# Kernel optimization log

Hardware: AMD Instinct MI355X
Metric: run time of the kernel (lower is better)

The kernel has to match this reference:

```python
import jax, jax.numpy as jnp
import numpy as np

NUM_HOPS = 4
N_NODES = 50000
N_EDGES = 500000
D = 128
H1 = 256
INIT_A, INIT_B = -0.01, 0.01


def _mlp(x, w1, b1, w2, b2):
    # Linear -> ReLU -> Linear -> ReLU (Dropout is identity in eval mode)
    h = jax.nn.relu(x @ w1 + b1)
    return jax.nn.relu(h @ w2 + b2)


def _uniform(key, shape):
    return jax.random.uniform(key, shape, jnp.float32, INIT_A, INIT_B)


def setup_inputs() -> dict:
    key = jax.random.key(0)
    ks = jax.random.split(key, 40)
    inp = {
        "batch_token": jax.random.normal(ks[0], (N_NODES, D), jnp.float32),
        "edge_p_node": jax.random.randint(ks[1], (N_EDGES,), 0, N_NODES),
        "edge_c_node": jax.random.randint(ks[2], (N_EDGES,), 0, N_NODES),
        "edge_p_indicate": jax.random.uniform(ks[3], (N_EDGES,), jnp.float32),
        "edge_c_indicate": jax.random.uniform(ks[4], (N_EDGES,), jnp.float32),
        "p_mask": jax.random.uniform(ks[5], (N_NODES,), jnp.float32),
        "c_mask": jax.random.uniform(ks[6], (N_NODES,), jnp.float32),
        "start_token": jax.random.normal(ks[7], (D,), jnp.float32),
        "end_token": jax.random.normal(ks[8], (D,), jnp.float32),
    }
    # MLP_V: D -> H1 -> D ; MLP_E: 1 -> H1 -> D ; MLP_p/c/aggr: 3D -> H1 -> D
    k = 9
    for name, din in (("V", D), ("E", 1), ("P", 3 * D), ("C", 3 * D), ("A", 3 * D)):
        inp[name + "w1"] = _uniform(ks[k], (din, H1)); k += 1
        inp[name + "b1"] = _uniform(ks[k], (H1,)); k += 1
        inp[name + "w2"] = _uniform(ks[k], (H1, D)); k += 1
        inp[name + "b2"] = _uniform(ks[k], (D,)); k += 1
    return inp


def reference(batch_token, edge_p_node, edge_c_node, edge_p_indicate,
              edge_c_indicate, p_mask, c_mask, start_token, end_token,
              Vw1, Vb1, Vw2, Vb2, Ew1, Eb1, Ew2, Eb2,
              Pw1, Pb1, Pw2, Pb2, Cw1, Cb1, Cw2, Cb2,
              Aw1, Ab1, Aw2, Ab2):
    n = batch_token.shape[0]
    h = _mlp(batch_token, Vw1, Vb1, Vw2, Vb2)  # [N, D]
    edge_p = _mlp(edge_p_indicate[:, None], Ew1, Eb1, Ew2, Eb2)  # [E, D]
    edge_c = _mlp(edge_c_indicate[:, None], Ew1, Eb1, Ew2, Eb2)  # [E, D]
    ones_e = jnp.ones((edge_p_node.shape[0],), jnp.float32)
    cnt_p = jnp.clip(jax.ops.segment_sum(ones_e, edge_p_node, num_segments=n), 1.0)
    cnt_c = jnp.clip(jax.ops.segment_sum(ones_e, edge_c_node, num_segments=n), 1.0)
    for _ in range(NUM_HOPS - 1):
        hp = h[edge_p_node]  # [E, D]
        hc = h[edge_c_node]  # [E, D]
        s_p = _mlp(jnp.concatenate([hc, hp, edge_p], -1), Pw1, Pb1, Pw2, Pb2)
        s_c = _mlp(jnp.concatenate([hp, hc, edge_c], -1), Cw1, Cb1, Cw2, Cb2)
        s_p = jax.ops.segment_sum(s_p, edge_p_node, num_segments=n) / cnt_p[:, None]
        s_c = jax.ops.segment_sum(s_c, edge_c_node, num_segments=n) / cnt_c[:, None]
        s_p = s_p + p_mask[:, None] * start_token
        s_c = s_c + c_mask[:, None] * end_token
        x_aggr = jnp.concatenate([h, s_p, s_c], -1)  # [N, 3D]
        h = jax.nn.relu(h + _mlp(x_aggr, Aw1, Ab1, Aw2, Ab2))
    return h
```

## Files before the change

### kernel.cpp

```cpp
#include <hip/hip_runtime.h>
#include <hip/hip_bf16.h>
#include <cstdint>
#include <cstddef>
#include <cmath>

typedef __bf16 bf16;
typedef bf16 bf16x8 __attribute__((ext_vector_type(8)));
typedef float f32x4 __attribute__((ext_vector_type(4)));

#define D_DIM 128
#define NB 32
#define EB 128
#define TS 136
#define XS 264
#define SRS 132
#define AS 392

__device__ __forceinline__ f32x4 mfma16(bf16x8 a, bf16x8 b, f32x4 c) {
  return __builtin_amdgcn_mfma_f32_16x16x32_bf16(a, b, c, 0, 0, 0);
}

__device__ __forceinline__ int clampi(int v, int hi) {
  return v < 0 ? 0 : (v > hi ? hi : v);
}

__device__ __forceinline__ void stage16(const float* __restrict__ src, bf16* dst) {
  bf16 tmp[16];
#pragma unroll
  for (int q = 0; q < 4; ++q) {
    f32x4 f = ((const f32x4*)src)[q];
#pragma unroll
    for (int j = 0; j < 4; ++j) tmp[q * 4 + j] = (bf16)f[j];
  }
  *(bf16x8*)dst = *(bf16x8*)tmp;
  *(bf16x8*)(dst + 8) = *(bf16x8*)(tmp + 8);
}

template <int NSEG>
__device__ __forceinline__ void mlp_layer1(const bf16* s0, const bf16* s1, const bf16* s2,
                                           const int S,
                                           const bf16* __restrict__ W1t,
                                           const float* __restrict__ B1,
                                           bf16* x2, const int lane, const int w) {
  const int col = lane & 15, quad = lane >> 4;
  const int K = NSEG * 128;
  f32x4 acc[2][4] = {};
  const bf16* segs[3] = {s0, s1, s2};
#pragma unroll
  for (int sg = 0; sg < NSEG; ++sg) {
    const bf16* xl = segs[sg];
#pragma unroll
    for (int kk = 0; kk < 128; kk += 32) {
      const int k0 = sg * 128 + kk;
      bf16x8 a0 = *(const bf16x8*)&xl[col * S + kk + quad * 8];
      bf16x8 a1 = *(const bf16x8*)&xl[(col + 16) * S + kk + quad * 8];
#pragma unroll
      for (int nt = 0; nt < 4; ++nt) {
        bf16x8 b = *(const bf16x8*)(W1t + (size_t)(w * 64 + nt * 16 + col) * K + k0 + quad * 8);
        acc[0][nt] = mfma16(a0, b, acc[0][nt]);
        acc[1][nt] = mfma16(a1, b, acc[1][nt]);
      }
    }
  }
#pragma unroll
  for (int nt = 0; nt < 4; ++nt) {
    const int n = w * 64 + nt * 16 + col;
    const float b1 = B1[n];
#pragma unroll
    for (int mt = 0; mt < 2; ++mt)
#pragma unroll
      for (int i = 0; i < 4; ++i) {
        float v = acc[mt][nt][i] + b1;
        x2[(mt * 16 + quad * 4 + i) * XS + n] = (bf16)(v > 0.f ? v : 0.f);
      }
  }
}

__device__ __forceinline__ void mlp_layer2(const bf16* x2, const bf16* __restrict__ W2t,
                                           const int lane, const int w, f32x4 acc2[2][2]) {
  const int col = lane & 15, quad = lane >> 4;
#pragma unroll
  for (int k0 = 0; k0 < 256; k0 += 32) {
    bf16x8 a0 = *(const bf16x8*)&x2[col * XS + k0 + quad * 8];
    bf16x8 a1 = *(const bf16x8*)&x2[(col + 16) * XS + k0 + quad * 8];
#pragma unroll
    for (int nt = 0; nt < 2; ++nt) {
      bf16x8 b = *(const bf16x8*)(W2t + (size_t)(w * 32 + nt * 16 + col) * 256 + k0 + quad * 8);
      acc2[0][nt] = mfma16(a0, b, acc2[0][nt]);
      acc2[1][nt] = mfma16(a1, b, acc2[1][nt]);
    }
  }
}

__device__ __forceinline__ void emit_z(const bf16* x, const int S,
                                       const bf16* __restrict__ Pw1t,
                                       const bf16* __restrict__ Cw1t,
                                       bf16* __restrict__ Zbuf,
                                       const int r0, const int N,
                                       const int lane, const int w) {
  const int col = lane & 15, quad = lane >> 4;
  const bf16* base = ((w & 2) ? Cw1t : Pw1t) + (w & 1) * 128;
  bf16* out = Zbuf + (size_t)w * ((size_t)N * 256);
#pragma unroll
  for (int half = 0; half < 2; ++half) {
    f32x4 acc[2][8] = {};
#pragma unroll
    for (int kc = 0; kc < 4; ++kc) {
      bf16x8 a0 = *(const bf16x8*)&x[col * S + kc * 32 + quad * 8];
      bf16x8 a1 = *(const bf16x8*)&x[(col + 16) * S + kc * 32 + quad * 8];
#pragma unroll
      for (int nt = 0; nt < 8; ++nt) {
        const int n = half * 128 + nt * 16 + col;
        bf16x8 b = *(const bf16x8*)(base + (size_t)n * 384 + kc * 32 + quad * 8);
        acc[0][nt] = mfma16(a0, b, acc[0][nt]);
        acc[1][nt] = mfma16(a1, b, acc[1][nt]);
      }
    }
#pragma unroll
    for (int nt = 0; nt < 8; ++nt) {
      const int n = half * 128 + nt * 16 + col;
#pragma unroll
      for (int mt = 0; mt < 2; ++mt)
#pragma unroll
        for (int i = 0; i < 4; ++i) {
          int g = r0 + mt * 16 + quad * 4 + i;
          if (g < N) out[(size_t)g * 256 + n] = (bf16)acc[mt][nt][i];
        }
    }
  }
}


__global__ void transpose_kernel(const float* __restrict__ in, bf16* __restrict__ out,
                                 int K, int N) {
  int k = blockIdx.x * blockDim.x + threadIdx.x;
  int n = blockIdx.y;
  if (k < K) out[(size_t)n * K + k] = (bf16)in[(size_t)k * N + n];
}

__global__ void count_kernel(const int* __restrict__ epn, const int* __restrict__ ecn,
                             int* cntp, int* cntc, int E, int N) {
  int i = blockIdx.x * blockDim.x + threadIdx.x;
  if (i < E) {
    atomicAdd(&cntp[clampi(epn[i], N - 1)], 1);
    atomicAdd(&cntc[clampi(ecn[i], N - 1)], 1);
  }
}

__global__ void inv_kernel(const int* __restrict__ cntp, const int* __restrict__ cntc,
                           float* invp, float* invc, int N) {
  int i = blockIdx.x * blockDim.x + threadIdx.x;
  if (i < N) {
    invp[i] = 1.f / fmaxf((float)cntp[i], 1.f);
    invc[i] = 1.f / fmaxf((float)cntc[i], 1.f);
  }
}

__global__ void scan_pair_kernel(const int* __restrict__ cntp, const int* __restrict__ cntc,
                                 int* __restrict__ offp, int* __restrict__ offc, int n) {
  const int* cnt = blockIdx.x ? cntc : cntp;
  int* offs = blockIdx.x ? offc : offp;
  __shared__ int buf[1024];
  __shared__ int carry;
  const int t = threadIdx.x;
  if (t == 0) carry = 0;
  __syncthreads();
  for (int base = 0; base < n; base += 1024) {
    int v = (base + t < n) ? cnt[base + t] : 0;
    buf[t] = v;
    __syncthreads();
    for (int d = 1; d < 1024; d <<= 1) {
      int add = (t >= d) ? buf[t - d] : 0;
      __syncthreads();
      buf[t] += add;
      __syncthreads();
    }
    if (base + t < n) offs[base + t] = carry + buf[t] - v;
    __syncthreads();
    if (t == 1023) carry += buf[1023];
    __syncthreads();
  }
}

__global__ void scatter_kernel(const int* __restrict__ epn, const int* __restrict__ ecn,
                               const int* __restrict__ offp, const int* __restrict__ offc,
                               int* curp, int* curc, int* sortp, int* sortc, int E, int N) {
  int i = blockIdx.x * blockDim.x + threadIdx.x;
  if (i < E) {
    int p = clampi(epn[i], N - 1);
    sortp[offp[p] + atomicAdd(&curp[p], 1)] = i;
    int c = clampi(ecn[i], N - 1);
    sortc[offc[c] + atomicAdd(&curc[c], 1)] = i;
  }
}


__global__ __launch_bounds__(256) void emlp_table_kernel(
    const float* __restrict__ Ew1, const float* __restrict__ Eb1,
    const float* __restrict__ Ew2, const float* __restrict__ Eb2,
    float* __restrict__ ts_out, float* __restrict__ Atab, float* __restrict__ Btab) {
  __shared__ float s_tk[256], s_w[256], s_b[256];
  __shared__ int s_k[256];
  __shared__ float sA[256], sB[256];
  const int j = blockIdx.x;
  const int t = threadIdx.x;
  float w = Ew1[t], b = Eb1[t];
  float tk = (w != 0.f) ? (-b / w) : INFINITY;
  s_tk[t] = tk; s_w[t] = w; s_b[t] = b;
  __syncthreads();
  int rank = 0;
  for (int u = 0; u < 256; ++u) {
    float tu = s_tk[u];
    if (tu < tk || (tu == tk && u < t)) ++rank;
  }
  s_k[rank] = t;
  if (j == 0) ts_out[rank] = tk;
  float w2own = Ew2[(size_t)t * 128 + j];
  bool act = (w < 0.f || (w == 0.f && b > 0.f));
  sA[t] = act ? w * w2own : 0.f;
  sB[t] = act ? b * w2own : 0.f;
  __syncthreads();
  for (int d = 128; d > 0; d >>= 1) {
    if (t < d) { sA[t] += sA[t + d]; sB[t] += sB[t + d]; }
    __syncthreads();
  }
  const float baseA = sA[0], baseB = sB[0];
  __syncthreads();
  int k = s_k[t];
  float wk = s_w[k], bk = s_b[k];
  float dA = 0.f, dB = 0.f;
  if (wk != 0.f) {
    float w2 = Ew2[(size_t)k * 128 + j];
    float sgn = wk > 0.f ? 1.f : -1.f;
    dA = sgn * wk * w2;
    dB = sgn * bk * w2;
  }
  sA[t] = dA; sB[t] = dB;
  __syncthreads();
  for (int d = 1; d < 256; d <<= 1) {
    float aA = (t >= d) ? sA[t - d] : 0.f;
    float aB = (t >= d) ? sB[t - d] : 0.f;
    __syncthreads();
    sA[t] += aA; sB[t] += aB;
    __syncthreads();
  }
  const float eb2 = Eb2[j];
  if (t == 0) { Atab[j] = baseA; Btab[j] = baseB + eb2; }
  Atab[(size_t)(t + 1) * 128 + j] = baseA + sA[t];
  Btab[(size_t)(t + 1) * 128 + j] = baseB + sB[t] + eb2;
}


__global__ __launch_bounds__(256, 3) void node_v_kernel(
    const float* __restrict__ bt, const bf16* __restrict__ W1t, const float* __restrict__ B1,
    const bf16* __restrict__ W2t, const float* __restrict__ B2,
    const bf16* __restrict__ Pw1t, const bf16* __restrict__ Cw1t,
    bf16* __restrict__ Zbuf, float* __restrict__ hout, int N) {
  __shared__ __attribute__((aligned(16))) bf16 x[NB * TS];
  __shared__ __attribute__((aligned(16))) bf16 x2[NB * XS];
  const int t = threadIdx.x;
  const int r0 = blockIdx.x * NB;
  {
    const int r = t >> 3, c0 = (t & 7) * 16;
    int g = r0 + r; if (g >= N) g = N - 1;
    stage16(bt + (size_t)g * D_DIM + c0, &x[r * TS + c0]);
  }
  __syncthreads();
  const int lane = t & 63, w = t >> 6, col = lane & 15, quad = lane >> 4;
  mlp_layer1<1>(x, x, x, TS, W1t, B1, x2, lane, w);
  __syncthreads();
  f32x4 acc2[2][2] = {};
  mlp_layer2(x2, W2t, lane, w, acc2);
  __syncthreads();
#pragma unroll
  for (int nt = 0; nt < 2; ++nt) {
    const int n = w * 32 + nt * 16 + col;
    const float b2 = B2[n];
#pragma unroll
    for (int mt = 0; mt < 2; ++mt)
#pragma unroll
      for (int i = 0; i < 4; ++i) {
        int m = mt * 16 + quad * 4 + i;
        int g = r0 + m;
        float v = acc2[mt][nt][i] + b2;
        v = v > 0.f ? v : 0.f;
        x[m * TS + n] = (bf16)v;
        if (g < N) hout[(size_t)g * D_DIM + n] = v;
      }
  }
  __syncthreads();
  emit_z(x, TS, Pw1t, Cw1t, Zbuf, r0, N, lane, w);
}


__global__ __launch_bounds__(1024, 8) void edge_side_kernel(
    const bf16* __restrict__ Zbuf,
    const float* __restrict__ epi, const float* __restrict__ eci,
    const int* __restrict__ epn, const int* __restrict__ ecn,
    const int* __restrict__ sortp, const int* __restrict__ sortc,
    const float* __restrict__ ets, const float* __restrict__ Atab,
    const float* __restrict__ Btab,
    const bf16* __restrict__ Pw1t, const float* __restrict__ Pb1,
    const bf16* __restrict__ Pw2t, const float* __restrict__ Pb2,
    const bf16* __restrict__ Cw1t, const float* __restrict__ Cb1,
    const bf16* __restrict__ Cw2t, const float* __restrict__ Cb2,
    float* __restrict__ accp, float* __restrict__ accc, int E, int N) {
  const int side = blockIdx.y;
  const size_t NZ = (size_t)N * 256;
  const bf16* ZO     = Zbuf + (size_t)(side * 2 + 0) * NZ;
  const bf16* ZW     = Zbuf + (size_t)(side * 2 + 1) * NZ;
  const float* ei    = side ? eci : epi;
  const int* own_n   = side ? ecn : epn;
  const int* oth_n   = side ? epn : ecn;
  const int* sorted  = side ? sortc : sortp;
  const bf16* W1c    = (side ? Cw1t : Pw1t) + 256;
  const float* B1    = side ? Cb1 : Pb1;
  const bf16* W2t    = side ? Cw2t : Pw2t;
  const float* B2    = side ? Cb2 : Pb2;
  float* acc         = side ? accc : accp;

  __shared__ int s_own[EB], s_oth[EB];
  __shared__ float s_x[EB];
  __shared__ float s_ts[256];
  __shared__ __attribute__((aligned(16))) char ubuf[EB * TS * 2 * 2];
  bf16* feat = (bf16*)ubuf;
  bf16* xzh  = (bf16*)(ubuf + EB * TS * 2);
  float* sred = (float*)ubuf;

  const int t = threadIdx.x;
  const int e0 = blockIdx.x * EB;
  if (t < 256) s_ts[t] = ets[t];
  if (t < EB) {
    int e = e0 + t;
    if (e < E) {
      int id = clampi(sorted[e], E - 1);
      s_own[t] = clampi(own_n[id], N - 1);
      s_oth[t] = clampi(oth_n[id], N - 1);
      s_x[t] = ei[id];
    } else {
      s_own[t] = -1; s_oth[t] = 0; s_x[t] = 0.f;
    }
  }
  __syncthreads();

  const int lane = t & 63, w = t >> 6, col = lane & 15, quad = lane >> 4;
  const int zr = t >> 3, zc = (t & 7) * 16;

  const bf16* zo_row;
  const bf16* zw_row;
  bf16x8 va[2];
  {
    int ro = s_oth[zr];
    int rw = s_own[zr]; if (rw < 0) rw = 0;
    zo_row = ZO + (size_t)ro * 256;
    zw_row = ZW + (size_t)rw * 256;
#pragma unroll
    for (int q = 0; q < 2; ++q) va[q] = *(const bf16x8*)(zo_row + zc + q * 8);
  }

  {
    const float xv = s_x[zr];
    int lo = 0, hi = 256;
#pragma unroll
    for (int it = 0; it < 8; ++it) {
      int mid = (lo + hi) >> 1;
      if (s_ts[mid] < xv) lo = mid + 1; else hi = mid;
    }
    const float* Ar = Atab + (size_t)lo * 128 + zc;
    const float* Br = Btab + (size_t)lo * 128 + zc;
#pragma unroll
    for (int q = 0; q < 2; ++q) {
      f32x4 a0 = *(const f32x4*)(Ar + q * 8);
      f32x4 a1 = *(const f32x4*)(Ar + q * 8 + 4);
      f32x4 b0 = *(const f32x4*)(Br + q * 8);
      f32x4 b1v = *(const f32x4*)(Br + q * 8 + 4);
      bf16 o[8];
#pragma unroll
      for (int j = 0; j < 4; ++j) {
        float v0 = fmaf(xv, a0[j], b0[j]);
        float v1 = fmaf(xv, a1[j], b1v[j]);
        o[j] = (bf16)(v0 > 0.f ? v0 : 0.f);
        o[4 + j] = (bf16)(v1 > 0.f ? v1 : 0.f);
      }
      *(bf16x8*)&feat[zr * TS + zc + q * 8] = *(bf16x8*)o;
    }
  }

  {
#pragma unroll
    for (int q = 0; q < 2; ++q) {
      bf16x8 b = *(const bf16x8*)(zw_row + zc + q * 8);
      bf16 o[8];
#pragma unroll
      for (int j = 0; j < 8; ++j) o[j] = (bf16)((float)va[q][j] + (float)b[j]);
      *(bf16x8*)&xzh[zr * TS + zc + q * 8] = *(bf16x8*)o;
    }
  }
  __syncthreads();

#pragma unroll
  for (int q = 0; q < 2; ++q) va[q] = *(const bf16x8*)(zo_row + 128 + zc + q * 8);

  f32x4 acc2[4];
#pragma unroll
  for (int g = 0; g < 4; ++g) acc2[g] = (f32x4){0.f, 0.f, 0.f, 0.f};

  const int nh = (w & 7) * 16 + col;
  const int rbase = (w >> 3) * 64;

  {
    f32x4 acc1[4] = {};
#pragma unroll
    for (int kc = 0; kc < 4; ++kc) {
      bf16x8 b = *(const bf16x8*)(W1c + (size_t)nh * 384 + kc * 32 + quad * 8);
#pragma unroll
      for (int g = 0; g < 4; ++g) {
        bf16x8 afr = *(const bf16x8*)&feat[(rbase + g * 16 + col) * TS + kc * 32 + quad * 8];
        acc1[g] = mfma16(afr, b, acc1[g]);
      }
    }
    const float b1v = B1[nh];
#pragma unroll
    for (int g = 0; g < 4; ++g)
#pragma unroll
      for (int i = 0; i < 4; ++i) {
        const int m = rbase + g * 16 + quad * 4 + i;
        float v = acc1[g][i] + b1v + (float)xzh[m * TS + nh];
        xzh[m * TS + nh] = (bf16)(v > 0.f ? v : 0.f);
      }
  }
  __syncthreads();
#pragma unroll
  for (int kc = 0; kc < 4; ++kc) {
    bf16x8 b = *(const bf16x8*)(W2t + (size_t)nh * 256 + kc * 32 + quad * 8);
#pragma unroll
    for (int g = 0; g < 4; ++g) {
      bf16x8 afr = *(const bf16x8*)&xzh[(rbase + g * 16 + col) * TS + kc * 32 + quad * 8];
      acc2[g] = mfma16(afr, b, acc2[g]);
    }
  }
  __syncthreads();

  {
#pragma unroll
    for (int q = 0; q < 2; ++q) {
      bf16x8 b = *(const bf16x8*)(zw_row + 128 + zc + q * 8);
      bf16 o[8];
#pragma unroll
      for (int j = 0; j < 8; ++j) o[j] = (bf16)((float)va[q][j] + (float)b[j]);
      *(bf16x8*)&xzh[zr * TS + zc + q * 8] = *(bf16x8*)o;
    }
  }
  __syncthreads();

  {
    f32x4 acc1[4] = {};
#pragma unroll
    for (int kc = 0; kc < 4; ++kc) {
      bf16x8 b = *(const bf16x8*)(W1c + (size_t)(128 + nh) * 384 + kc * 32 + quad * 8);
#pragma unroll
      for (int g = 0; g < 4; ++g) {
        bf16x8 afr = *(const bf16x8*)&feat[(rbase + g * 16 + col) * TS + kc * 32 + quad * 8];
        acc1[g] = mfma16(afr, b, acc1[g]);
      }
    }
    const float b1v = B1[128 + nh];
#pragma unroll
    for (int g = 0; g < 4; ++g)
#pragma unroll
      for (int i = 0; i < 4; ++i) {
        const int m = rbase + g * 16 + quad * 4 + i;
        float v = acc1[g][i] + b1v + (float)xzh[m * TS + nh];
        xzh[m * TS + nh] = (bf16)(v > 0.f ? v : 0.f);
      }
  }
  __syncthreads();
#pragma unroll
  for (int kc = 0; kc < 4; ++kc) {
    bf16x8 b = *(const bf16x8*)(W2t + (size_t)nh * 256 + 128 + kc * 32 + quad * 8);
#pragma unroll
    for (int g = 0; g < 4; ++g) {
      bf16x8 afr = *(const bf16x8*)&xzh[(rbase + g * 16 + col) * TS + kc * 32 + quad * 8];
      acc2[g] = mfma16(afr, b, acc2[g]);
    }
  }
  __syncthreads();

  {
    const float b2 = B2[nh];
#pragma unroll
    for (int g = 0; g < 4; ++g)
#pragma unroll
      for (int i = 0; i < 4; ++i) {
        float v = acc2[g][i] + b2;
        sred[(rbase + g * 16 + quad * 4 + i) * SRS + nh] = v > 0.f ? v : 0.f;
      }
  }
  __syncthreads();
  {
    const int c = t & 127;
    const int rlo = (t >> 7) * 16;
    float run = 0.f;
    int cur = s_own[rlo];
    for (int r = rlo; r < rlo + 16; ++r) {
      int k = s_own[r];
      if (k != cur) {
        if (cur >= 0)
          __hip_atomic_fetch_add(&acc[(size_t)cur * D_DIM + c], run,
                                 __ATOMIC_RELAXED, __HIP_MEMORY_SCOPE_AGENT);
        run = 0.f;
        cur = k;
      }
      run += sred[r * SRS + c];
    }
    if (cur >= 0)
      __hip_atomic_fetch_add(&acc[(size_t)cur * D_DIM + c], run,
                             __ATOMIC_RELAXED, __HIP_MEMORY_SCOPE_AGENT);
  }
}


__global__ __launch_bounds__(256, 3) void node_a_kernel(
    const float* __restrict__ h, const float* __restrict__ accp, const float* __restrict__ accc,
    const float* __restrict__ invp, const float* __restrict__ invc,
    const float* __restrict__ pmask, const float* __restrict__ cmask,
    const float* __restrict__ stok, const float* __restrict__ etok,
    const bf16* __restrict__ W1t, const float* __restrict__ B1,
    const bf16* __restrict__ W2t, const float* __restrict__ B2,
    const bf16* __restrict__ Pw1t, const bf16* __restrict__ Cw1t,
    bf16* __restrict__ Zbuf, int emitZ,
    float* __restrict__ hout, int N) {
  __shared__ __attribute__((aligned(16))) bf16 x[NB * AS];
  __shared__ __attribute__((aligned(16))) bf16 x2[NB * XS];
  const int t = threadIdx.x;
  const int r0 = blockIdx.x * NB;
  {
    const int r = t >> 3, c0 = (t & 7) * 16;
    int g = r0 + r; if (g >= N) g = N - 1;
    stage16(h + (size_t)g * D_DIM + c0, &x[r * AS + c0]);
  }
  {
    const int j = t;
    for (int r = 0; r < NB; ++r) {
      int g = r0 + r; if (g >= N) g = N - 1;
      float v;
      if (j < 128)
        v = accp[(size_t)g * D_DIM + j] * invp[g] + pmask[g] * stok[j];
      else {
        int jj = j - 128;
        v = accc[(size_t)g * D_DIM + jj] * invc[g] + cmask[g] * etok[jj];
      }
      x[r * AS + 128 + j] = (bf16)v;
    }
  }
  __syncthreads();
  const int lane = t & 63, w = t >> 6, col = lane & 15, quad = lane >> 4;
  mlp_layer1<3>(x, x + 128, x + 256, AS, W1t, B1, x2, lane, w);
  __syncthreads();
  f32x4 acc2[2][2] = {};
  mlp_layer2(x2, W2t, lane, w, acc2);
  __syncthreads();
#pragma unroll
  for (int nt = 0; nt < 2; ++nt) {
    const int n = w * 32 + nt * 16 + col;
    const float b2 = B2[n];
#pragma unroll
    for (int mt = 0; mt < 2; ++mt)
#pragma unroll
      for (int i = 0; i < 4; ++i) {
        int m = mt * 16 + quad * 4 + i;
        int g = r0 + m;
        int gc = g < N ? g : N - 1;
        float mlpv = acc2[mt][nt][i] + b2;
        mlpv = mlpv > 0.f ? mlpv : 0.f;
        float v = h[(size_t)gc * D_DIM + n] + mlpv;
        v = v > 0.f ? v : 0.f;
        x[m * AS + n] = (bf16)v;
        if (g < N) hout[(size_t)g * D_DIM + n] = v;
      }
  }
  if (emitZ) {
    __syncthreads();
    emit_z(x, AS, Pw1t, Cw1t, Zbuf, r0, N, lane, w);
  }
}


extern "C" void kernel_launch(void* const* d_in, const int* in_sizes, int n_in,
                              void* d_out, int out_size, void* d_ws, size_t ws_size,
                              hipStream_t stream) {
  const float* batch_token = (const float*)d_in[0];
  const int* epn = (const int*)d_in[1];
  const int* ecn = (const int*)d_in[2];
  const float* epi = (const float*)d_in[3];
  const float* eci = (const float*)d_in[4];
  const float* pmask = (const float*)d_in[5];
  const float* cmask = (const float*)d_in[6];
  const float* stok = (const float*)d_in[7];
  const float* etok = (const float*)d_in[8];
  const float *Vw1 = (const float*)d_in[9], *Vb1 = (const float*)d_in[10],
              *Vw2 = (const float*)d_in[11], *Vb2 = (const float*)d_in[12];
  const float *Ew1 = (const float*)d_in[13], *Eb1 = (const float*)d_in[14],
              *Ew2 = (const float*)d_in[15], *Eb2 = (const float*)d_in[16];
  const float *Pw1 = (const float*)d_in[17], *Pb1 = (const float*)d_in[18],
              *Pw2 = (const float*)d_in[19], *Pb2 = (const float*)d_in[20];
  const float *Cw1 = (const float*)d_in[21], *Cb1 = (const float*)d_in[22],
              *Cw2 = (const float*)d_in[23], *Cb2 = (const float*)d_in[24];
  const float *Aw1 = (const float*)d_in[25], *Ab1 = (const float*)d_in[26],
              *Aw2 = (const float*)d_in[27], *Ab2 = (const float*)d_in[28];
  const int N = in_sizes[5];
  const int E = in_sizes[1];

  char* ws = (char*)d_ws;
  size_t off = 0;
  auto alloc = [&](size_t bytes) {
    size_t o = off;
    off += (bytes + 511) & ~(size_t)511;
    return o;
  };
  float* accp = (float*)(ws + alloc((size_t)N * D_DIM * 4));
  float* accc = (float*)(ws + alloc((size_t)N * D_DIM * 4));
  bf16* Zbuf = (bf16*)(ws + alloc((size_t)4 * N * 256 * 2));
  float* invp = (float*)(ws + alloc((size_t)N * 4));
  float* invc = (float*)(ws + alloc((size_t)N * 4));
  int* cntp = (int*)(ws + alloc((size_t)N * 4));
  int* cntc = (int*)(ws + alloc((size_t)N * 4));
  int* offp = (int*)(ws + alloc((size_t)N * 4));
  int* offc = (int*)(ws + alloc((size_t)N * 4));
  int* curp = (int*)(ws + alloc((size_t)N * 4));
  int* curc = (int*)(ws + alloc((size_t)N * 4));
  int* sortp = (int*)(ws + alloc((size_t)E * 4));
  int* sortc = (int*)(ws + alloc((size_t)E * 4));
  bf16* Vw1t = (bf16*)(ws + alloc(128 * 256 * 2));
  bf16* Pw1t = (bf16*)(ws + alloc(384 * 256 * 2));
  bf16* Cw1t = (bf16*)(ws + alloc(384 * 256 * 2));
  bf16* Aw1t = (bf16*)(ws + alloc(384 * 256 * 2));
  bf16* Vw2t = (bf16*)(ws + alloc(256 * 128 * 2));
  bf16* Pw2t = (bf16*)(ws + alloc(256 * 128 * 2));
  bf16* Cw2t = (bf16*)(ws + alloc(256 * 128 * 2));
  bf16* Aw2t = (bf16*)(ws + alloc(256 * 128 * 2));
  float* ets  = (float*)(ws + alloc(256 * 4));
  float* Atab = (float*)(ws + alloc((size_t)257 * 128 * 4));
  float* Btab = (float*)(ws + alloc((size_t)257 * 128 * 4));
  float* hbuf = (float*)d_out;
  (void)ws_size; (void)n_in; (void)out_size;

  const dim3 blk(256);
  transpose_kernel<<<dim3(1, 256), blk, 0, stream>>>(Vw1, Vw1t, 128, 256);
  transpose_kernel<<<dim3(2, 256), blk, 0, stream>>>(Pw1, Pw1t, 384, 256);
  transpose_kernel<<<dim3(2, 256), blk, 0, stream>>>(Cw1, Cw1t, 384, 256);
  transpose_kernel<<<dim3(2, 256), blk, 0, stream>>>(Aw1, Aw1t, 384, 256);
  transpose_kernel<<<dim3(1, 128), blk, 0, stream>>>(Vw2, Vw2t, 256, 128);
  transpose_kernel<<<dim3(1, 128), blk, 0, stream>>>(Pw2, Pw2t, 256, 128);
  transpose_kernel<<<dim3(1, 128), blk, 0, stream>>>(Cw2, Cw2t, 256, 128);
  transpose_kernel<<<dim3(1, 128), blk, 0, stream>>>(Aw2, Aw2t, 256, 128);

  emlp_table_kernel<<<dim3(128), dim3(256), 0, stream>>>(Ew1, Eb1, Ew2, Eb2, ets, Atab, Btab);

  const size_t cntbytes = (size_t)((char*)(cntc + N) - (char*)cntp);
  hipMemsetAsync(cntp, 0, cntbytes, stream);
  count_kernel<<<dim3((E + 255) / 256), blk, 0, stream>>>(epn, ecn, cntp, cntc, E, N);
  inv_kernel<<<dim3((N + 255) / 256), blk, 0, stream>>>(cntp, cntc, invp, invc, N);
  scan_pair_kernel<<<dim3(2), dim3(1024), 0, stream>>>(cntp, cntc, offp, offc, N);
  const size_t curbytes = (size_t)((char*)(curc + N) - (char*)curp);
  hipMemsetAsync(curp, 0, curbytes, stream);
  scatter_kernel<<<dim3((E + 255) / 256), blk, 0, stream>>>(epn, ecn, offp, offc,
                                                            curp, curc, sortp, sortc, E, N);

  const int nblocks = (N + NB - 1) / NB;
  const int eblocks = (E + EB - 1) / EB;

  node_v_kernel<<<dim3(nblocks), blk, 0, stream>>>(
      batch_token, Vw1t, Vb1, Vw2t, Vb2, Pw1t, Cw1t, Zbuf, hbuf, N);

  const size_t accbytes = (size_t)((char*)(accc + (size_t)N * D_DIM) - (char*)accp);
  for (int hop = 0; hop < 3; ++hop) {
    hipMemsetAsync(accp, 0, accbytes, stream);
    edge_side_kernel<<<dim3(eblocks, 2), dim3(1024), 0, stream>>>(
        Zbuf, epi, eci, epn, ecn, sortp, sortc, ets, Atab, Btab,
        Pw1t, Pb1, Pw2t, Pb2, Cw1t, Cb1, Cw2t, Cb2, accp, accc, E, N);
    node_a_kernel<<<dim3(nblocks), blk, 0, stream>>>(
        hbuf, accp, accc, invp, invc, pmask, cmask, stok, etok,
        Aw1t, Ab1, Aw2t, Ab2, Pw1t, Cw1t, Zbuf, (hop < 2) ? 1 : 0, hbuf, N);
  }
}
```

Measured before the change: 1.992 ms.

## Presort edge data, alias node-kernel LDS, fold accumulator zeroing into node kernel

```diff
diff --git a/kernel.cpp b/kernel.cpp
--- a/kernel.cpp
+++ b/kernel.cpp
@@ -37,14 +37,13 @@
 }
 
 template <int NSEG>
-__device__ __forceinline__ void mlp_layer1(const bf16* s0, const bf16* s1, const bf16* s2,
-                                           const int S,
-                                           const bf16* __restrict__ W1t,
-                                           const float* __restrict__ B1,
-                                           bf16* x2, const int lane, const int w) {
+__device__ __forceinline__ void mlp_layer1_compute(const bf16* s0, const bf16* s1,
+                                                   const bf16* s2, const int S,
+                                                   const bf16* __restrict__ W1t,
+                                                   f32x4 acc[2][4],
+                                                   const int lane, const int w) {
   const int col = lane & 15, quad = lane >> 4;
   const int K = NSEG * 128;
-  f32x4 acc[2][4] = {};
   const bf16* segs[3] = {s0, s1, s2};
 #pragma unroll
   for (int sg = 0; sg < NSEG; ++sg) {
@@ -62,6 +61,12 @@
       }
     }
   }
+}
+
+__device__ __forceinline__ void mlp_layer1_store(f32x4 acc[2][4],
+                                                 const float* __restrict__ B1,
+                                                 bf16* x2, const int lane, const int w) {
+  const int col = lane & 15, quad = lane >> 4;
 #pragma unroll
   for (int nt = 0; nt < 4; ++nt) {
     const int n = w * 64 + nt * 16 + col;
@@ -183,14 +188,19 @@
 }
 
 __global__ void scatter_kernel(const int* __restrict__ epn, const int* __restrict__ ecn,
+                               const float* __restrict__ epi, const float* __restrict__ eci,
                                const int* __restrict__ offp, const int* __restrict__ offc,
-                               int* curp, int* curc, int* sortp, int* sortc, int E, int N) {
+                               int* curp, int* curc,
+                               int* ownp_s, int* othp_s, float* xp_s,
+                               int* ownc_s, int* othc_s, float* xc_s, int E, int N) {
   int i = blockIdx.x * blockDim.x + threadIdx.x;
   if (i < E) {
     int p = clampi(epn[i], N - 1);
-    sortp[offp[p] + atomicAdd(&curp[p], 1)] = i;
     int c = clampi(ecn[i], N - 1);
-    sortc[offc[c] + atomicAdd(&curc[c], 1)] = i;
+    int pp = offp[p] + atomicAdd(&curp[p], 1);
+    ownp_s[pp] = p; othp_s[pp] = c; xp_s[pp] = epi[i];
+    int pc = offc[c] + atomicAdd(&curc[c], 1);
+    ownc_s[pc] = c; othc_s[pc] = p; xc_s[pc] = eci[i];
   }
 }
 
@@ -251,13 +261,15 @@
 }
 
 
-__global__ __launch_bounds__(256, 3) void node_v_kernel(
+__global__ __launch_bounds__(256, 4) void node_v_kernel(
     const float* __restrict__ bt, const bf16* __restrict__ W1t, const float* __restrict__ B1,
     const bf16* __restrict__ W2t, const float* __restrict__ B2,
     const bf16* __restrict__ Pw1t, const bf16* __restrict__ Cw1t,
     bf16* __restrict__ Zbuf, float* __restrict__ hout, int N) {
-  __shared__ __attribute__((aligned(16))) bf16 x[NB * TS];
-  __shared__ __attribute__((aligned(16))) bf16 x2[NB * XS];
+  __shared__ __attribute__((aligned(16))) char ubuf[NB * XS * 2];
+  bf16* x = (bf16*)ubuf;
+  bf16* x2 = (bf16*)ubuf;
+  bf16* xh = (bf16*)ubuf;
   const int t = threadIdx.x;
   const int r0 = blockIdx.x * NB;
   {
@@ -267,7 +279,10 @@
   }
   __syncthreads();
   const int lane = t & 63, w = t >> 6, col = lane & 15, quad = lane >> 4;
-  mlp_layer1<1>(x, x, x, TS, W1t, B1, x2, lane, w);
+  f32x4 acc1[2][4] = {};
+  mlp_layer1_compute<1>(x, x, x, TS, W1t, acc1, lane, w);
+  __syncthreads();
+  mlp_layer1_store(acc1, B1, x2, lane, w);
   __syncthreads();
   f32x4 acc2[2][2] = {};
   mlp_layer2(x2, W2t, lane, w, acc2);
@@ -284,20 +299,21 @@
         int g = r0 + m;
         float v = acc2[mt][nt][i] + b2;
         v = v > 0.f ? v : 0.f;
-        x[m * TS + n] = (bf16)v;
+        xh[m * TS + n] = (bf16)v;
         if (g < N) hout[(size_t)g * D_DIM + n] = v;
       }
   }
   __syncthreads();
-  emit_z(x, TS, Pw1t, Cw1t, Zbuf, r0, N, lane, w);
+  emit_z(xh, TS, Pw1t, Cw1t, Zbuf, r0, N, lane, w);
 }
 
 
 __global__ __launch_bounds__(1024, 8) void edge_side_kernel(
     const bf16* __restrict__ Zbuf,
-    const float* __restrict__ epi, const float* __restrict__ eci,
-    const int* __restrict__ epn, const int* __restrict__ ecn,
-    const int* __restrict__ sortp, const int* __restrict__ sortc,
+    const int* __restrict__ ownp_s, const int* __restrict__ othp_s,
+    const float* __restrict__ xp_s,
+    const int* __restrict__ ownc_s, const int* __restrict__ othc_s,
+    const float* __restrict__ xc_s,
     const float* __restrict__ ets, const float* __restrict__ Atab,
     const float* __restrict__ Btab,
     const bf16* __restrict__ Pw1t, const float* __restrict__ Pb1,
@@ -309,10 +325,9 @@
   const size_t NZ = (size_t)N * 256;
   const bf16* ZO     = Zbuf + (size_t)(side * 2 + 0) * NZ;
   const bf16* ZW     = Zbuf + (size_t)(side * 2 + 1) * NZ;
-  const float* ei    = side ? eci : epi;
-  const int* own_n   = side ? ecn : epn;
-  const int* oth_n   = side ? epn : ecn;
-  const int* sorted  = side ? sortc : sortp;
+  const int* owns    = side ? ownc_s : ownp_s;
+  const int* oths    = side ? othc_s : othp_s;
+  const float* xs    = side ? xc_s : xp_s;
   const bf16* W1c    = (side ? Cw1t : Pw1t) + 256;
   const float* B1    = side ? Cb1 : Pb1;
   const bf16* W2t    = side ? Cw2t : Pw2t;
@@ -333,10 +348,9 @@
   if (t < EB) {
     int e = e0 + t;
     if (e < E) {
-      int id = clampi(sorted[e], E - 1);
-      s_own[t] = clampi(own_n[id], N - 1);
-      s_oth[t] = clampi(oth_n[id], N - 1);
-      s_x[t] = ei[id];
+      s_own[t] = owns[e];
+      s_oth[t] = oths[e];
+      s_x[t] = xs[e];
     } else {
       s_own[t] = -1; s_oth[t] = 0; s_x[t] = 0.f;
     }
@@ -520,18 +534,20 @@
 }
 
 
-__global__ __launch_bounds__(256, 3) void node_a_kernel(
-    const float* __restrict__ h, const float* __restrict__ accp, const float* __restrict__ accc,
+__global__ __launch_bounds__(256, 4) void node_a_kernel(
+    const float* __restrict__ h, float* __restrict__ accp, float* __restrict__ accc,
     const float* __restrict__ invp, const float* __restrict__ invc,
     const float* __restrict__ pmask, const float* __restrict__ cmask,
     const float* __restrict__ stok, const float* __restrict__ etok,
     const bf16* __restrict__ W1t, const float* __restrict__ B1,
     const bf16* __restrict__ W2t, const float* __restrict__ B2,
     const bf16* __restrict__ Pw1t, const bf16* __restrict__ Cw1t,
-    bf16* __restrict__ Zbuf, int emitZ,
+    bf16* __restrict__ Zbuf, int emitZ, int zeroAcc,
     float* __restrict__ hout, int N) {
-  __shared__ __attribute__((aligned(16))) bf16 x[NB * AS];
-  __shared__ __attribute__((aligned(16))) bf16 x2[NB * XS];
+  __shared__ __attribute__((aligned(16))) char ubuf[NB * AS * 2];
+  bf16* x = (bf16*)ubuf;
+  bf16* x2 = (bf16*)ubuf;
+  bf16* xh = (bf16*)ubuf;
   const int t = threadIdx.x;
   const int r0 = blockIdx.x * NB;
   {
@@ -544,18 +560,25 @@
     for (int r = 0; r < NB; ++r) {
       int g = r0 + r; if (g >= N) g = N - 1;
       float v;
-      if (j < 128)
-        v = accp[(size_t)g * D_DIM + j] * invp[g] + pmask[g] * stok[j];
-      else {
+      if (j < 128) {
+        float* pa = &accp[(size_t)g * D_DIM + j];
+        v = *pa * invp[g] + pmask[g] * stok[j];
+        if (zeroAcc) *pa = 0.f;
+      } else {
         int jj = j - 128;
-        v = accc[(size_t)g * D_DIM + jj] * invc[g] + cmask[g] * etok[jj];
+        float* pa = &accc[(size_t)g * D_DIM + jj];
+        v = *pa * invc[g] + cmask[g] * etok[jj];
+        if (zeroAcc) *pa = 0.f;
       }
       x[r * AS + 128 + j] = (bf16)v;
     }
   }
   __syncthreads();
   const int lane = t & 63, w = t >> 6, col = lane & 15, quad = lane >> 4;
-  mlp_layer1<3>(x, x + 128, x + 256, AS, W1t, B1, x2, lane, w);
+  f32x4 acc1[2][4] = {};
+  mlp_layer1_compute<3>(x, x + 128, x + 256, AS, W1t, acc1, lane, w);
+  __syncthreads();
+  mlp_layer1_store(acc1, B1, x2, lane, w);
   __syncthreads();
   f32x4 acc2[2][2] = {};
   mlp_layer2(x2, W2t, lane, w, acc2);
@@ -575,13 +598,13 @@
         mlpv = mlpv > 0.f ? mlpv : 0.f;
         float v = h[(size_t)gc * D_DIM + n] + mlpv;
         v = v > 0.f ? v : 0.f;
-        x[m * AS + n] = (bf16)v;
+        xh[m * TS + n] = (bf16)v;
         if (g < N) hout[(size_t)g * D_DIM + n] = v;
       }
   }
   if (emitZ) {
     __syncthreads();
-    emit_z(x, AS, Pw1t, Cw1t, Zbuf, r0, N, lane, w);
+    emit_z(xh, TS, Pw1t, Cw1t, Zbuf, r0, N, lane, w);
   }
 }
 
@@ -629,8 +652,12 @@
   int* offc = (int*)(ws + alloc((size_t)N * 4));
   int* curp = (int*)(ws + alloc((size_t)N * 4));
   int* curc = (int*)(ws + alloc((size_t)N * 4));
-  int* sortp = (int*)(ws + alloc((size_t)E * 4));
-  int* sortc = (int*)(ws + alloc((size_t)E * 4));
+  int* ownp_s = (int*)(ws + alloc((size_t)E * 4));
+  int* othp_s = (int*)(ws + alloc((size_t)E * 4));
+  float* xp_s = (float*)(ws + alloc((size_t)E * 4));
+  int* ownc_s = (int*)(ws + alloc((size_t)E * 4));
+  int* othc_s = (int*)(ws + alloc((size_t)E * 4));
+  float* xc_s = (float*)(ws + alloc((size_t)E * 4));
   bf16* Vw1t = (bf16*)(ws + alloc(128 * 256 * 2));
   bf16* Pw1t = (bf16*)(ws + alloc(384 * 256 * 2));
   bf16* Cw1t = (bf16*)(ws + alloc(384 * 256 * 2));
@@ -664,8 +691,9 @@
   scan_pair_kernel<<<dim3(2), dim3(1024), 0, stream>>>(cntp, cntc, offp, offc, N);
   const size_t curbytes = (size_t)((char*)(curc + N) - (char*)curp);
   hipMemsetAsync(curp, 0, curbytes, stream);
-  scatter_kernel<<<dim3((E + 255) / 256), blk, 0, stream>>>(epn, ecn, offp, offc,
-                                                            curp, curc, sortp, sortc, E, N);
+  scatter_kernel<<<dim3((E + 255) / 256), blk, 0, stream>>>(
+      epn, ecn, epi, eci, offp, offc, curp, curc,
+      ownp_s, othp_s, xp_s, ownc_s, othc_s, xc_s, E, N);
 
   const int nblocks = (N + NB - 1) / NB;
   const int eblocks = (E + EB - 1) / EB;
@@ -674,13 +702,14 @@
       batch_token, Vw1t, Vb1, Vw2t, Vb2, Pw1t, Cw1t, Zbuf, hbuf, N);
 
   const size_t accbytes = (size_t)((char*)(accc + (size_t)N * D_DIM) - (char*)accp);
+  hipMemsetAsync(accp, 0, accbytes, stream);
   for (int hop = 0; hop < 3; ++hop) {
-    hipMemsetAsync(accp, 0, accbytes, stream);
     edge_side_kernel<<<dim3(eblocks, 2), dim3(1024), 0, stream>>>(
-        Zbuf, epi, eci, epn, ecn, sortp, sortc, ets, Atab, Btab,
+        Zbuf, ownp_s, othp_s, xp_s, ownc_s, othc_s, xc_s, ets, Atab, Btab,
         Pw1t, Pb1, Pw2t, Pb2, Cw1t, Cb1, Cw2t, Cb2, accp, accc, E, N);
     node_a_kernel<<<dim3(nblocks), blk, 0, stream>>>(
         hbuf, accp, accc, invp, invc, pmask, cmask, stok, etok,
-        Aw1t, Ab1, Aw2t, Ab2, Pw1t, Cw1t, Zbuf, (hop < 2) ? 1 : 0, hbuf, N);
-  }
-}
+        Aw1t, Ab1, Aw2t, Ab2, Pw1t, Cw1t, Zbuf, (hop < 2) ? 1 : 0, (hop < 2) ? 1 : 0,
+        hbuf, N);
+  }
+}
```

Measured after the change: 2.061 ms. 3.5% more time.
